# Kernel optimization log

Measured on AMD Instinct MI355X. Metric: run time of the kernel, lower is better.

The kernel has to match this reference:

```python
import jax, jax.numpy as jnp
import numpy as np
from jax import lax

V, E, NL, NS, DC, EX = 32000, 1024, 4, 16, 4, 2
DI = EX * E          # 2048 inner dim
DTR = E // 16        # 64 dt_rank
BSZ, L = 2, 512
EPS = 1e-5


def setup_inputs() -> dict:
    key = jax.random.key(0)
    ks = jax.random.split(key, 12)
    s = 0.02
    emb = jax.random.normal(ks[0], (V, E), jnp.float32) * s
    ln_w = jnp.ones((NL, E), jnp.float32)
    ln_b = jnp.zeros((NL, E), jnp.float32)
    in_proj_w = jax.random.normal(ks[1], (NL, 2 * DI, E), jnp.float32) * s
    conv_w = jax.random.normal(ks[2], (NL, DI, DC), jnp.float32) * 0.1
    conv_b = jnp.zeros((NL, DI), jnp.float32)
    x_proj_w = jax.random.normal(ks[3], (NL, DTR + 2 * NS, DI), jnp.float32) * s
    dt_proj_w = jax.random.normal(ks[4], (NL, DI, DTR), jnp.float32) * s
    dt_proj_b = jax.random.normal(ks[5], (NL, DI), jnp.float32) * 0.1
    # canonical S4D-real init: A[d,n] = n+1  ->  A_log = log(A)
    A_log = jnp.log(jnp.tile(jnp.arange(1, NS + 1, dtype=jnp.float32)[None, None, :], (NL, DI, 1)))
    D_param = jnp.ones((NL, DI), jnp.float32)
    out_proj_w = jax.random.normal(ks[6], (NL, E, DI), jnp.float32) * s
    fln_w = jnp.ones((E,), jnp.float32)
    fln_b = jnp.zeros((E,), jnp.float32)
    input_ids = jax.random.randint(ks[7], (BSZ, L), 0, V, jnp.int64)
    targets = jax.random.randint(ks[8], (BSZ, L), 0, V, jnp.int64)
    return dict(input_ids=input_ids, targets=targets, emb=emb, ln_w=ln_w, ln_b=ln_b,
                in_proj_w=in_proj_w, conv_w=conv_w, conv_b=conv_b, x_proj_w=x_proj_w,
                dt_proj_w=dt_proj_w, dt_proj_b=dt_proj_b, A_log=A_log, D_param=D_param,
                out_proj_w=out_proj_w, fln_w=fln_w, fln_b=fln_b)


def _layer_norm(x, w, b):
    mu = x.mean(-1, keepdims=True)
    var = ((x - mu) ** 2).mean(-1, keepdims=True)
    return (x - mu) * lax.rsqrt(var + EPS) * w + b


def _mamba_block(x, in_w, cw, cb, xw, dtw, dtb, a_log, d_par, ow):
    # x: (B,L,E)
    xz = jnp.einsum('ble,fe->blf', x, in_w)          # (B,L,2*DI)
    u, res = jnp.split(xz, 2, axis=-1)               # each (B,L,DI)
    # causal depthwise conv1d, kernel width DC (left pad DC-1)
    u_pad = jnp.pad(u, ((0, 0), (DC - 1, 0), (0, 0)))
    u_conv = sum(cw[:, k] * u_pad[:, k:k + u.shape[1], :] for k in range(DC))
    u = jax.nn.silu(u_conv + cb)
    x_dbl = jnp.einsum('bld,fd->blf', u, xw)         # (B,L,DTR+2*NS)
    dt = x_dbl[..., :DTR]
    Bm = x_dbl[..., DTR:DTR + NS]                    # (B,L,NS)
    Cm = x_dbl[..., DTR + NS:]                       # (B,L,NS)
    delta = jax.nn.softplus(jnp.einsum('blr,dr->bld', dt, dtw) + dtb)  # (B,L,DI)
    A = -jnp.exp(a_log)                              # (DI,NS)
    dA = jnp.exp(delta[..., None] * A)               # (B,L,DI,NS)
    dBu = delta[..., None] * Bm[:, :, None, :] * u[..., None]

    def step(h, inp):
        dA_t, dBu_t, C_t = inp
        h = dA_t * h + dBu_t                         # (B,DI,NS)
        y = jnp.einsum('bdn,bn->bd', h, C_t)
        return h, y

    h0 = jnp.zeros((x.shape[0], DI, NS), x.dtype)
    _, ys = lax.scan(step, h0, (dA.transpose(1, 0, 2, 3), dBu.transpose(1, 0, 2, 3), Cm.transpose(1, 0, 2)))
    y = ys.transpose(1, 0, 2) + u * d_par            # (B,L,DI)
    y = y * jax.nn.silu(res)
    return jnp.einsum('bld,ed->ble', y, ow)


def reference(input_ids, targets, emb, ln_w, ln_b, in_proj_w, conv_w, conv_b,
              x_proj_w, dt_proj_w, dt_proj_b, A_log, D_param, out_proj_w, fln_w, fln_b):
    x = emb[input_ids]                               # (B,L,E)
    for l in range(NL):
        h = _layer_norm(x, ln_w[l], ln_b[l])
        h = _mamba_block(h, in_proj_w[l], conv_w[l], conv_b[l], x_proj_w[l],
                         dt_proj_w[l], dt_proj_b[l], A_log[l], D_param[l], out_proj_w[l])
        x = x + h
    x = _layer_norm(x, fln_w, fln_b)
    logits = jnp.einsum('ble,ve->blv', x, emb)       # tied lm_head
    logp = jax.nn.log_softmax(logits, axis=-1)
    valid = targets != -1
    safe_t = jnp.where(valid, targets, 0)
    nll = -jnp.take_along_axis(logp, safe_t[..., None], axis=-1)[..., 0]
    loss = jnp.where(valid, nll, 0.0).mean()
    return logits, loss
```

## Files before the change

kernel.cpp:

```cpp
#include <hip/hip_runtime.h>
#include <cstdint>
#include <cstddef>

#define L_SEQ 512
#define NBATCH 2
#define NTOK 1024
#define E_DIM 1024
#define V_DIM 32000
#define DI_DIM 2048
#define NS_DIM 16
#define DTR_DIM 64
#define DC_DIM 4
#define NL_DIM 4
#define NC 8
#define LC (L_SEQ / NC)

typedef __bf16 bf16;
typedef __bf16 bf16x8 __attribute__((ext_vector_type(8)));
typedef __bf16 bf16x4 __attribute__((ext_vector_type(4)));
typedef float  f32x4  __attribute__((ext_vector_type(4)));

__device__ __forceinline__ void gload_lds16(const void* g, void* l)
{
    __builtin_amdgcn_global_load_lds((const __attribute__((address_space(1))) uint32_t*)g,
                                     (__attribute__((address_space(3))) uint32_t*)l, 16, 0, 0);
}

__device__ __forceinline__ float softplusf(float z)
{
    return fmaxf(z, 0.0f) + log1pf(expf(-fabsf(z)));
}

__global__ void cast_f32_to_bf16(const float* __restrict__ in, bf16* __restrict__ out, int n4)
{
    int stride = gridDim.x * blockDim.x;
    for (int i = blockIdx.x * blockDim.x + threadIdx.x; i < n4; i += stride) {
        f32x4 v = ((const f32x4*)in)[i];
        bf16x4 o;
        o[0] = (bf16)v[0]; o[1] = (bf16)v[1]; o[2] = (bf16)v[2]; o[3] = (bf16)v[3];
        ((bf16x4*)out)[i] = o;
    }
}

__global__ void cast3_kernel(const float* __restrict__ a, bf16* __restrict__ oa, int na4,
                             const float* __restrict__ b, bf16* __restrict__ ob, int nb4,
                             const float* __restrict__ c, bf16* __restrict__ oc, int nc4)
{
    int stride = gridDim.x * blockDim.x;
    int tot = na4 + nb4 + nc4;
    for (int i = blockIdx.x * blockDim.x + threadIdx.x; i < tot; i += stride) {
        const float* src; bf16* dst; int k = i;
        if (k < na4) { src = a; dst = oa; }
        else if ((k -= na4) < nb4) { src = b; dst = ob; }
        else { k -= nb4; src = c; dst = oc; }
        f32x4 v = ((const f32x4*)src)[k];
        bf16x4 o;
        o[0] = (bf16)v[0]; o[1] = (bf16)v[1]; o[2] = (bf16)v[2]; o[3] = (bf16)v[3];
        ((bf16x4*)dst)[k] = o;
    }
}

__global__ void embed_kernel(const int* __restrict__ ids, const float* __restrict__ emb,
                             float* __restrict__ x)
{
    int t = blockIdx.x;
    int id = ids[t];
    ((f32x4*)(x + (size_t)t * E_DIM))[threadIdx.x] =
        ((const f32x4*)(emb + (size_t)id * E_DIM))[threadIdx.x];
}

__global__ void ln_kernel(const float* __restrict__ x, const float* __restrict__ w,
                          const float* __restrict__ b, bf16* __restrict__ out)
{
    int t = blockIdx.x;
    int tid = threadIdx.x;
    f32x4 v = ((const f32x4*)(x + (size_t)t * E_DIM))[tid];
    float s  = v[0] + v[1] + v[2] + v[3];
    float sq = v[0]*v[0] + v[1]*v[1] + v[2]*v[2] + v[3]*v[3];
#pragma unroll
    for (int off = 1; off < 64; off <<= 1) { s += __shfl_xor(s, off); sq += __shfl_xor(sq, off); }
    __shared__ float ps[4], pq[4];
    if ((tid & 63) == 0) { ps[tid >> 6] = s; pq[tid >> 6] = sq; }
    __syncthreads();
    float S  = ps[0] + ps[1] + ps[2] + ps[3];
    float SQ = pq[0] + pq[1] + pq[2] + pq[3];
    float mu  = S * (1.0f / E_DIM);
    float var = SQ * (1.0f / E_DIM) - mu * mu;
    float rs  = rsqrtf(var + 1e-5f);
    f32x4 wv = ((const f32x4*)w)[tid];
    f32x4 bv = ((const f32x4*)b)[tid];
    bf16x4 o;
#pragma unroll
    for (int i = 0; i < 4; ++i) o[i] = (bf16)((v[i] - mu) * rs * wv[i] + bv[i]);
    ((bf16x4*)(out + (size_t)t * E_DIM))[tid] = o;
}

template<int BM, int BN, int BK, int MODE, int SK>
__global__ __launch_bounds__(256) void gemm_bt(const bf16* __restrict__ A, const bf16* __restrict__ B,
                                               void* __restrict__ Cv, int K,
                                               int lda, int ldb, int ldc,
                                               const float* __restrict__ bias,
                                               int RB, int CB, int CBpad)
{
    int pid = blockIdx.x;
    int per = RB * CBpad;
    int sk  = pid / per;
    int rem = pid - sk * per;
    int xcd = rem & 7;
    int j   = rem >> 3;
    int cpx = CBpad >> 3;
    int rb  = j % RB;
    int cb  = xcd * cpx + j / RB;
    if (cb >= CB) return;
    int kseg = K / SK;
    int kbeg = sk * kseg;
    int kend = kbeg + kseg;

    __shared__ __align__(16) bf16 As[BM * BK];
    __shared__ __align__(16) bf16 Bs[BN * BK];
    int tid  = threadIdx.x;
    int lane = tid & 63;
    int wid  = tid >> 6;
    int wr = wid >> 1, wc = wid & 1;
    int li = lane & 15, lg = lane >> 4;
    const bf16* Ablk = A + (size_t)(rb * BM) * lda;
    const bf16* Bblk = B + (size_t)(cb * BN) * ldb;
    constexpr int MR   = BM / 32;
    constexpr int NR   = BN / 32;
    constexpr int SEGS = BK / 8;
    constexpr int AOPS = BM * SEGS;
    constexpr int TOT  = (BM + BN) * SEGS;
    f32x4 acc[MR][NR] = {};
    for (int k0 = kbeg; k0 < kend; k0 += BK) {
        __syncthreads();
#pragma unroll
        for (int it = 0; it < TOT / 256; ++it) {
            int wbase = it * 256 + wid * 64;
            int idx   = wbase + lane;
            if (wbase < AOPS) {
                int row = idx / SEGS, seg = idx % SEGS;
                gload_lds16(Ablk + (size_t)row * lda + k0 + seg * 8, As + (size_t)wbase * 8);
            } else {
                int bb  = wbase - AOPS;
                int bi  = bb + lane;
                int row = bi / SEGS, seg = bi % SEGS;
                gload_lds16(Bblk + (size_t)row * ldb + k0 + seg * 8, Bs + (size_t)bb * 8);
            }
        }
        __syncthreads();
#pragma unroll
        for (int kk = 0; kk < BK / 32; ++kk) {
            bf16x8 af[MR], bfr[NR];
#pragma unroll
            for (int m = 0; m < MR; ++m)
                af[m]  = *(const bf16x8*)&As[(wr * (BM/2) + m * 16 + li) * BK + kk * 32 + lg * 8];
#pragma unroll
            for (int n = 0; n < NR; ++n)
                bfr[n] = *(const bf16x8*)&Bs[(wc * (BN/2) + n * 16 + li) * BK + kk * 32 + lg * 8];
#pragma unroll
            for (int m = 0; m < MR; ++m)
#pragma unroll
                for (int n = 0; n < NR; ++n)
                    acc[m][n] = __builtin_amdgcn_mfma_f32_16x16x32_bf16(af[m], bfr[n], acc[m][n], 0, 0, 0);
        }
    }
    int row0 = rb * BM + wr * (BM/2);
    int col0 = cb * BN + wc * (BN/2);
    float* Cf = (float*)Cv;
    bf16*  Cb = (bf16*)Cv;
#pragma unroll
    for (int m = 0; m < MR; ++m) {
#pragma unroll
        for (int n = 0; n < NR; ++n) {
            int r = row0 + m * 16 + lg * 4;
            int c = col0 + n * 16 + li;
#pragma unroll
            for (int q = 0; q < 4; ++q) {
                float v = acc[m][n][q];
                if (MODE == 0) {
                    Cf[(size_t)(r + q) * ldc + c] = v;
                } else if (MODE == 2) {
                    Cb[(size_t)(r + q) * ldc + c] = (bf16)softplusf(v + bias[c]);
                } else if (MODE == 4) {
                    Cb[(size_t)(r + q) * ldc + c] = (bf16)v;
                } else if (MODE == 5) {
                    atomicAdd(Cf + (size_t)(r + q) * ldc + c, v);
                }
            }
        }
    }
}

template<int BM, int BN, int BK, int MODE, int SK = 1>
static void launch_gemm(const bf16* A, const bf16* B, void* C, int M, int N, int K,
                        int lda, int ldb, int ldc, const float* bias, hipStream_t stream)
{
    int RB = M / BM;
    int CB = (N + BN - 1) / BN;
    int CBpad = (CB + 7) & ~7;
    gemm_bt<BM, BN, BK, MODE, SK><<<RB * CBpad * SK, 256, 0, stream>>>(A, B, C, K, lda, ldb, ldc,
                                                                       bias, RB, CB, CBpad);
}

__global__ __launch_bounds__(256) void cxk_kernel(
        const bf16* __restrict__ xz, const float* __restrict__ cw,
        const float* __restrict__ cb, const float* __restrict__ xw,
        float* __restrict__ xdbl, bf16* __restrict__ dt_bf, bf16* __restrict__ u_bf)
{
    int t0  = blockIdx.x * 4;
    int bb  = t0 >> 9;
    int tid = threadIdx.x;
    int f   = tid & 127;
    int ks  = tid >> 7;
    __shared__ __align__(16) float sxz[7][256];
    __shared__ __align__(16) float su[4][256];
    __shared__ float pacc[4][128];
    float acc[4] = {0, 0, 0, 0};
    for (int kc = 0; kc < DI_DIM; kc += 256) {
        __syncthreads();
        if (tid < 224) {
            int row = tid >> 5, c8 = (tid & 31) * 8;
            int tr = t0 - 3 + row;
            float vals[8] = {0, 0, 0, 0, 0, 0, 0, 0};
            if (tr >= bb * L_SEQ) {
                bf16x8 v = *(const bf16x8*)&xz[(size_t)tr * (2 * DI_DIM) + kc + c8];
#pragma unroll
                for (int jj = 0; jj < 8; ++jj) vals[jj] = (float)v[jj];
            }
#pragma unroll
            for (int jj = 0; jj < 8; ++jj) sxz[row][c8 + jj] = vals[jj];
        }
        __syncthreads();
        {
            int c = tid;
            const float* cwp = cw + (size_t)(kc + c) * DC_DIM;
            float w0 = cwp[0], w1 = cwp[1], w2 = cwp[2], w3 = cwp[3];
            float bs = cb[kc + c];
#pragma unroll
            for (int tt = 0; tt < 4; ++tt) {
                float a = bs + w0 * sxz[tt][c] + w1 * sxz[tt + 1][c]
                             + w2 * sxz[tt + 2][c] + w3 * sxz[tt + 3][c];
                float uo = a / (1.0f + __expf(-a));
                su[tt][c] = uo;
                u_bf[(size_t)(t0 + tt) * DI_DIM + kc + c] = (bf16)uo;
            }
        }
        __syncthreads();
        if (f < 96) {
            int kb = ks * 128;
            for (int kk = kb; kk < kb + 128; kk += 4) {
                f32x4 wv = *(const f32x4*)&xw[(size_t)f * DI_DIM + kc + kk];
#pragma unroll
                for (int tt = 0; tt < 4; ++tt) {
                    f32x4 uv = *(f32x4*)&su[tt][kk];
                    acc[tt] += wv[0]*uv[0] + wv[1]*uv[1] + wv[2]*uv[2] + wv[3]*uv[3];
                }
            }
        }
    }
    if (ks == 1 && f < 96) {
#pragma unroll
        for (int tt = 0; tt < 4; ++tt) pacc[tt][f] = acc[tt];
    }
    __syncthreads();
    if (ks == 0 && f < 96) {
#pragma unroll
        for (int tt = 0; tt < 4; ++tt) {
            float v = acc[tt] + pacc[tt][f];
            xdbl[(size_t)(t0 + tt) * 96 + f] = v;
            if (f < 64) dt_bf[(size_t)(t0 + tt) * DTR_DIM + f] = (bf16)v;
        }
    }
}

__global__ __launch_bounds__(256) void scan_phase_a(
        const bf16* __restrict__ delta, const float* __restrict__ xdbl,
        const bf16* __restrict__ u_bf, const float* __restrict__ A_log,
        float* __restrict__ Pbuf, float* __restrict__ Sbuf)
{
    int tid = threadIdx.x;
    int c   = blockIdx.x & (NC - 1);
    int dblk= (blockIdx.x >> 3) & 127;
    int b   = blockIdx.x >> 10;
    int d0  = dblk << 4;
    int n = tid & 15, dl = tid >> 4;
    int d = d0 + dl;
    float Ac = -expf(A_log[(size_t)d * NS_DIM + n]);
    float h = 0.0f, P = 1.0f;
    __shared__ float s_dlt[32][16], s_u[32][16], s_B[32][16];
    int tt0 = tid >> 4, cc = tid & 15;
    int tbase = b * L_SEQ + c * LC;
    for (int t0 = 0; t0 < LC; t0 += 32) {
        __syncthreads();
#pragma unroll
        for (int jj = 0; jj < 2; ++jj) {
            int tt = jj * 16 + tt0;
            size_t trow = (size_t)(tbase + t0 + tt);
            s_dlt[tt][cc] = (float)delta[trow * DI_DIM + d0 + cc];
            s_u[tt][cc]   = (float)u_bf[trow * DI_DIM + d0 + cc];
            s_B[tt][cc]   = xdbl[trow * 96 + 64 + cc];
        }
        __syncthreads();
#pragma unroll
        for (int t = 0; t < 32; ++t) {
            float dlt = s_dlt[t][dl];
            float dA  = __expf(dlt * Ac);
            h = fmaf(dA, h, dlt * s_B[t][n] * s_u[t][dl]);
            P *= dA;
        }
    }
    size_t oi = (((size_t)(b * NC + c) * DI_DIM) + d) * NS_DIM + n;
    Pbuf[oi] = P;
    Sbuf[oi] = h;
}

__global__ __launch_bounds__(256) void scan_phase_c(
        const bf16* __restrict__ delta, const float* __restrict__ xdbl,
        const bf16* __restrict__ u_bf, const bf16* __restrict__ xz,
        const float* __restrict__ A_log, const float* __restrict__ D_par,
        const float* __restrict__ Pbuf, const float* __restrict__ Sbuf,
        bf16* __restrict__ y)
{
    int tid = threadIdx.x;
    int c   = blockIdx.x & (NC - 1);
    int dblk= (blockIdx.x >> 3) & 127;
    int b   = blockIdx.x >> 10;
    int d0  = dblk << 4;
    int n = tid & 15, dl = tid >> 4;
    int d = d0 + dl;
    float Ac = -expf(A_log[(size_t)d * NS_DIM + n]);
    float Dp = D_par[d];
    float h = 0.0f;
    for (int cp = 0; cp < c; ++cp) {
        size_t oi = (((size_t)(b * NC + cp) * DI_DIM) + d) * NS_DIM + n;
        h = fmaf(Pbuf[oi], h, Sbuf[oi]);
    }
    __shared__ float s_dlt[32][16], s_u[32][16], s_res[32][16], s_B[32][16], s_C[32][16];
    __shared__ bf16  s_y[32][16];
    int tt0 = tid >> 4, cc = tid & 15;
    int tbase = b * L_SEQ + c * LC;
    for (int t0 = 0; t0 < LC; t0 += 32) {
        __syncthreads();
#pragma unroll
        for (int jj = 0; jj < 2; ++jj) {
            int tt = jj * 16 + tt0;
            size_t trow = (size_t)(tbase + t0 + tt);
            s_dlt[tt][cc] = (float)delta[trow * DI_DIM + d0 + cc];
            s_u[tt][cc]   = (float)u_bf[trow * DI_DIM + d0 + cc];
            s_res[tt][cc] = (float)xz[trow * (2 * DI_DIM) + DI_DIM + d0 + cc];
            s_B[tt][cc]   = xdbl[trow * 96 + 64 + cc];
            s_C[tt][cc]   = xdbl[trow * 96 + 80 + cc];
        }
        __syncthreads();
#pragma unroll
        for (int t = 0; t < 32; ++t) {
            float dlt = s_dlt[t][dl];
            float uu  = s_u[t][dl];
            float dA  = __expf(dlt * Ac);
            float dBu = dlt * s_B[t][n] * uu;
            h = fmaf(dA, h, dBu);
            float yp = h * s_C[t][n];
            yp += __shfl_xor(yp, 1);
            yp += __shfl_xor(yp, 2);
            yp += __shfl_xor(yp, 4);
            yp += __shfl_xor(yp, 8);
            if (n == 0) {
                float res = s_res[t][dl];
                float yv  = fmaf(uu, Dp, yp) * (res / (1.0f + __expf(-res)));
                s_y[t][dl] = (bf16)yv;
            }
        }
        __syncthreads();
#pragma unroll
        for (int jj = 0; jj < 2; ++jj) {
            int tt = jj * 16 + tt0;
            size_t trow = (size_t)(tbase + t0 + tt);
            y[trow * DI_DIM + d0 + cc] = s_y[tt][cc];
        }
    }
}

__global__ void lse_nll_kernel(const float* __restrict__ logits, const int* __restrict__ targets,
                               float* __restrict__ lossp)
{
    int t = blockIdx.x, tid = threadIdx.x;
    const f32x4* row = (const f32x4*)(logits + (size_t)t * V_DIM);
    float m = -1e30f, s = 0.0f;
    for (int i = tid; i < V_DIM / 4; i += 256) {
        f32x4 v = row[i];
        float m4 = fmaxf(fmaxf(v[0], v[1]), fmaxf(v[2], v[3]));
        if (m4 > m) { s *= __expf(m - m4); m = m4; }
        s += __expf(v[0] - m) + __expf(v[1] - m) + __expf(v[2] - m) + __expf(v[3] - m);
    }
#pragma unroll
    for (int off = 1; off < 64; off <<= 1) {
        float mo = __shfl_xor(m, off), so = __shfl_xor(s, off);
        float nm = fmaxf(m, mo);
        s = s * __expf(m - nm) + so * __expf(mo - nm);
        m = nm;
    }
    __shared__ float pm[4], ps2[4];
    if ((tid & 63) == 0) { pm[tid >> 6] = m; ps2[tid >> 6] = s; }
    __syncthreads();
    if (tid == 0) {
        float M = fmaxf(fmaxf(pm[0], pm[1]), fmaxf(pm[2], pm[3]));
        float S = ps2[0] * __expf(pm[0] - M) + ps2[1] * __expf(pm[1] - M)
                + ps2[2] * __expf(pm[2] - M) + ps2[3] * __expf(pm[3] - M);
        int tg = targets[t];
        if (tg >= 0) {
            float v = (M + logf(S)) - logits[(size_t)t * V_DIM + tg];
            atomicAdd(lossp, v * (1.0f / NTOK));
        }
    }
}

extern "C" void kernel_launch(void* const* d_in, const int* in_sizes, int n_in,
                              void* d_out, int out_size, void* d_ws, size_t ws_size,
                              hipStream_t stream)
{
    const int*   ids   = (const int*)d_in[0];
    const int*   tgt   = (const int*)d_in[1];
    const float* emb   = (const float*)d_in[2];
    const float* ln_w  = (const float*)d_in[3];
    const float* ln_b  = (const float*)d_in[4];
    const float* inw   = (const float*)d_in[5];
    const float* convw = (const float*)d_in[6];
    const float* convb = (const float*)d_in[7];
    const float* xw    = (const float*)d_in[8];
    const float* dtw   = (const float*)d_in[9];
    const float* dtb   = (const float*)d_in[10];
    const float* alog  = (const float*)d_in[11];
    const float* dpar  = (const float*)d_in[12];
    const float* outw  = (const float*)d_in[13];
    const float* flnw  = (const float*)d_in[14];
    const float* flnb  = (const float*)d_in[15];
    float* logits = (float*)d_out;
    float* lossp  = logits + (size_t)NTOK * V_DIM;

    const size_t INW_L  = (size_t)2 * DI_DIM * E_DIM;
    const size_t OUTW_L = (size_t)E_DIM * DI_DIM;
    const size_t DTW_L  = (size_t)DI_DIM * DTR_DIM;

    char* wsp = (char*)d_ws;
    size_t off = 0;
    auto alloc = [&](size_t bytes) -> void* {
        void* p = wsp + off;
        off += (bytes + 255) & ~(size_t)255;
        return p;
    };
    bf16*  emb_bf  = (bf16*)alloc((size_t)V_DIM * E_DIM * 2);
    float* x       = (float*)alloc((size_t)NTOK * E_DIM * 4);
    bf16*  h_bf    = (bf16*)alloc((size_t)NTOK * E_DIM * 2);
    bf16*  xzb     = (bf16*)alloc((size_t)NTOK * 2 * DI_DIM * 2);
    bf16*  u_bf    = (bf16*)alloc((size_t)NTOK * DI_DIM * 2);
    float* xdbl    = (float*)alloc((size_t)NTOK * 96 * 4);
    bf16*  dt_bf   = (bf16*)alloc((size_t)NTOK * DTR_DIM * 2);
    bf16*  deltab  = (bf16*)alloc((size_t)NTOK * DI_DIM * 2);
    bf16*  y_bf    = (bf16*)alloc((size_t)NTOK * DI_DIM * 2);
    bf16*  xf_bf   = (bf16*)alloc((size_t)NTOK * E_DIM * 2);
    float* Pbuf    = (float*)alloc((size_t)NBATCH * NC * DI_DIM * NS_DIM * 4);
    float* Sbuf    = (float*)alloc((size_t)NBATCH * NC * DI_DIM * NS_DIM * 4);
    size_t base = off;
    size_t big_need = base + (((size_t)NL_DIM * INW_L * 2 + 255) & ~(size_t)255)
                           + (((size_t)NL_DIM * OUTW_L * 2 + 255) & ~(size_t)255)
                           + (((size_t)NL_DIM * DTW_L * 2 + 255) & ~(size_t)255);
    bool big = (big_need <= ws_size);
    bf16* winl; bf16* woutl; bf16* wdtl;
    if (big) {
        winl  = (bf16*)alloc((size_t)NL_DIM * INW_L * 2);
        woutl = (bf16*)alloc((size_t)NL_DIM * OUTW_L * 2);
        wdtl  = (bf16*)alloc((size_t)NL_DIM * DTW_L * 2);
    } else {
        winl  = (bf16*)alloc(INW_L * 2);
        woutl = (bf16*)alloc(OUTW_L * 2);
        wdtl  = (bf16*)alloc(DTW_L * 2);
    }
    if (off > ws_size) return;

    hipMemsetAsync(lossp, 0, sizeof(float), stream);
    {
        int n4 = (int)((size_t)V_DIM * E_DIM / 4);
        cast_f32_to_bf16<<<4096, 256, 0, stream>>>(emb, emb_bf, n4);
    }
    if (big) {
        cast3_kernel<<<4096, 256, 0, stream>>>(
            inw,  winl,  (int)((size_t)NL_DIM * INW_L / 4),
            outw, woutl, (int)((size_t)NL_DIM * OUTW_L / 4),
            dtw,  wdtl,  (int)((size_t)NL_DIM * DTW_L / 4));
    }
    embed_kernel<<<NTOK, 256, 0, stream>>>(ids, emb, x);

    for (int l = 0; l < NL_DIM; ++l) {
        const bf16* wi = big ? winl  + (size_t)l * INW_L  : winl;
        const bf16* wo = big ? woutl + (size_t)l * OUTW_L : woutl;
        const bf16* wd = big ? wdtl  + (size_t)l * DTW_L  : wdtl;
        if (!big) {
            cast3_kernel<<<2048, 256, 0, stream>>>(
                inw  + (size_t)l * INW_L,  winl,  (int)(INW_L / 4),
                outw + (size_t)l * OUTW_L, woutl, (int)(OUTW_L / 4),
                dtw  + (size_t)l * DTW_L,  wdtl,  (int)(DTW_L / 4));
        }
        ln_kernel<<<NTOK, 256, 0, stream>>>(x, ln_w + l * E_DIM, ln_b + l * E_DIM, h_bf);
        launch_gemm<128, 64, 64, 4>(h_bf, wi, xzb, NTOK, 2 * DI_DIM, E_DIM,
                                    E_DIM, E_DIM, 2 * DI_DIM, nullptr, stream);
        cxk_kernel<<<NTOK / 4, 256, 0, stream>>>(
            xzb, convw + (size_t)l * DI_DIM * DC_DIM, convb + (size_t)l * DI_DIM,
            xw + (size_t)l * 96 * DI_DIM, xdbl, dt_bf, u_bf);
        launch_gemm<64, 64, 64, 2>(dt_bf, wd, deltab, NTOK, DI_DIM, DTR_DIM,
                                   DTR_DIM, DTR_DIM, DI_DIM, dtb + (size_t)l * DI_DIM, stream);
        scan_phase_a<<<NBATCH * (DI_DIM / 16) * NC, 256, 0, stream>>>(
            deltab, xdbl, u_bf, alog + (size_t)l * DI_DIM * NS_DIM, Pbuf, Sbuf);
        scan_phase_c<<<NBATCH * (DI_DIM / 16) * NC, 256, 0, stream>>>(
            deltab, xdbl, u_bf, xzb, alog + (size_t)l * DI_DIM * NS_DIM,
            dpar + (size_t)l * DI_DIM, Pbuf, Sbuf, y_bf);
        launch_gemm<128, 128, 64, 5, 4>(y_bf, wo, x, NTOK, E_DIM, DI_DIM,
                                        DI_DIM, DI_DIM, E_DIM, nullptr, stream);
    }
    ln_kernel<<<NTOK, 256, 0, stream>>>(x, flnw, flnb, xf_bf);
    launch_gemm<128, 128, 64, 0>(xf_bf, emb_bf, logits, NTOK, V_DIM, E_DIM,
                                 E_DIM, E_DIM, V_DIM, nullptr, stream);
    lse_nll_kernel<<<NTOK, 256, 0, stream>>>(logits, tgt, lossp);
}
```

Baseline: 857.9 us.

## Add dedicated 256x256-tile logits GEMM and shrink K-tile of layer GEMMs

Replaces the generic logits GEMM with a specialized 512-thread kernel that computes 256x256 output tiles. It uses double-buffered LDS staging via direct global-to-LDS loads, XOR swizzling, and a custom block-to-tile mapping over the 125 column blocks. The layer GEMMs switch their K tile from 64 to 32, which lowers LDS use and may raise occupancy at the cost of more loop iterations and syncs. The large tile gives more reuse per LDS load for the dominant vocab projection, but it needs 128 KB of LDS and many accumulator registers per thread.

```diff
diff --git a/kernel.cpp b/kernel.cpp
--- a/kernel.cpp
+++ b/kernel.cpp
@@ -200,6 +200,98 @@
     int CBpad = (CB + 7) & ~7;
     gemm_bt<BM, BN, BK, MODE, SK><<<RB * CBpad * SK, 256, 0, stream>>>(A, B, C, K, lda, ldb, ldc,
                                                                        bias, RB, CB, CBpad);
+}
+
+__global__ __launch_bounds__(512) void gemm256_logits(const bf16* __restrict__ A,
+                                                      const bf16* __restrict__ B,
+                                                      float* __restrict__ C)
+{
+    int pid = blockIdx.x;
+    int x = pid & 7, i = pid >> 3;
+    int cbq = (x < 5) ? 16 : 15;
+    int ci = i >> 2;
+    if (ci >= cbq) return;
+    int cb = (x < 5) ? x * 16 + ci : 80 + (x - 5) * 15 + ci;
+    int rb = i & 3;
+
+    __shared__ __align__(16) bf16 Abuf[2][256 * 64];
+    __shared__ __align__(16) bf16 Bbuf[2][256 * 64];
+    int tid  = threadIdx.x;
+    int lane = tid & 63, wid = tid >> 6;
+    int wr = wid >> 2, wc = wid & 3;
+    int li = lane & 15, lg = lane >> 4;
+    const bf16* Ablk = A + (size_t)(rb * 256) * E_DIM;
+    const bf16* Bblk = B + (size_t)(cb * 256) * E_DIM;
+
+    f32x4 acc[8][4] = {};
+
+    auto stage = [&](int buf, int k0) {
+#pragma unroll
+        for (int sw = 0; sw < 4; ++sw) {
+            int wb  = sw * 8192 + wid * 1024;
+            int y   = wb + lane * 16;
+            int row = y >> 7;
+            int colb = (y & 127) ^ ((row & 4) << 3);
+            gload_lds16(Ablk + (size_t)row * E_DIM + k0 + (colb >> 1),
+                        (char*)Abuf[buf] + wb);
+        }
+#pragma unroll
+        for (int sw = 0; sw < 4; ++sw) {
+            int wb  = sw * 8192 + wid * 1024;
+            int y   = wb + lane * 16;
+            int row = y >> 7;
+            int colb = (y & 127) ^ ((row & 4) << 3);
+            gload_lds16(Bblk + (size_t)row * E_DIM + k0 + (colb >> 1),
+                        (char*)Bbuf[buf] + wb);
+        }
+    };
+
+    stage(0, 0);
+    __syncthreads();
+    int cur = 0;
+    for (int t = 0; t < E_DIM / 64; ++t) {
+        if (t + 1 < E_DIM / 64) stage(cur ^ 1, (t + 1) * 64);
+        const char* Ab = (const char*)Abuf[cur];
+        const char* Bb = (const char*)Bbuf[cur];
+#pragma unroll
+        for (int kk = 0; kk < 2; ++kk) {
+            bf16x8 af[8], bfr[4];
+#pragma unroll
+            for (int m = 0; m < 8; ++m) {
+                int row = wr * 128 + m * 16 + li;
+                int ab  = ((row << 7) + kk * 64 + lg * 16) ^ ((li & 4) << 3);
+                af[m] = *(const bf16x8*)(Ab + ab);
+            }
+#pragma unroll
+            for (int n = 0; n < 4; ++n) {
+                int row = wc * 64 + n * 16 + li;
+                int bb  = ((row << 7) + kk * 64 + lg * 16) ^ ((li & 4) << 3);
+                bfr[n] = *(const bf16x8*)(Bb + bb);
+            }
+            __builtin_amdgcn_s_setprio(1);
+#pragma unroll
+            for (int m = 0; m < 8; ++m)
+#pragma unroll
+                for (int n = 0; n < 4; ++n)
+                    acc[m][n] = __builtin_amdgcn_mfma_f32_16x16x32_bf16(af[m], bfr[n], acc[m][n], 0, 0, 0);
+            __builtin_amdgcn_s_setprio(0);
+        }
+        __syncthreads();
+        cur ^= 1;
+    }
+    int row0 = rb * 256 + wr * 128;
+    int col0 = cb * 256 + wc * 64;
+#pragma unroll
+    for (int m = 0; m < 8; ++m) {
+#pragma unroll
+        for (int n = 0; n < 4; ++n) {
+            int r = row0 + m * 16 + lg * 4;
+            int c = col0 + n * 16 + li;
+#pragma unroll
+            for (int q = 0; q < 4; ++q)
+                C[(size_t)(r + q) * V_DIM + c] = acc[m][n][q];
+        }
+    }
 }
 
 __global__ __launch_bounds__(256) void cxk_kernel(
@@ -501,23 +593,22 @@
                 dtw  + (size_t)l * DTW_L,  wdtl,  (int)(DTW_L / 4));
         }
         ln_kernel<<<NTOK, 256, 0, stream>>>(x, ln_w + l * E_DIM, ln_b + l * E_DIM, h_bf);
-        launch_gemm<128, 64, 64, 4>(h_bf, wi, xzb, NTOK, 2 * DI_DIM, E_DIM,
+        launch_gemm<128, 64, 32, 4>(h_bf, wi, xzb, NTOK, 2 * DI_DIM, E_DIM,
                                     E_DIM, E_DIM, 2 * DI_DIM, nullptr, stream);
         cxk_kernel<<<NTOK / 4, 256, 0, stream>>>(
             xzb, convw + (size_t)l * DI_DIM * DC_DIM, convb + (size_t)l * DI_DIM,
             xw + (size_t)l * 96 * DI_DIM, xdbl, dt_bf, u_bf);
-        launch_gemm<64, 64, 64, 2>(dt_bf, wd, deltab, NTOK, DI_DIM, DTR_DIM,
+        launch_gemm<64, 64, 32, 2>(dt_bf, wd, deltab, NTOK, DI_DIM, DTR_DIM,
                                    DTR_DIM, DTR_DIM, DI_DIM, dtb + (size_t)l * DI_DIM, stream);
         scan_phase_a<<<NBATCH * (DI_DIM / 16) * NC, 256, 0, stream>>>(
             deltab, xdbl, u_bf, alog + (size_t)l * DI_DIM * NS_DIM, Pbuf, Sbuf);
         scan_phase_c<<<NBATCH * (DI_DIM / 16) * NC, 256, 0, stream>>>(
             deltab, xdbl, u_bf, xzb, alog + (size_t)l * DI_DIM * NS_DIM,
             dpar + (size_t)l * DI_DIM, Pbuf, Sbuf, y_bf);
-        launch_gemm<128, 128, 64, 5, 4>(y_bf, wo, x, NTOK, E_DIM, DI_DIM,
+        launch_gemm<128, 128, 32, 5, 4>(y_bf, wo, x, NTOK, E_DIM, DI_DIM,
                                         DI_DIM, DI_DIM, E_DIM, nullptr, stream);
     }
     ln_kernel<<<NTOK, 256, 0, stream>>>(x, flnw, flnb, xf_bf);
-    launch_gemm<128, 128, 64, 0>(xf_bf, emb_bf, logits, NTOK, V_DIM, E_DIM,
-                                 E_DIM, E_DIM, V_DIM, nullptr, stream);
+    gemm256_logits<<<512, 512, 0, stream>>>(xf_bf, emb_bf, logits);
     lse_nll_kernel<<<NTOK, 256, 0, stream>>>(logits, tgt, lossp);
 }
```

New measurement: 845.8 us. Within noise of the previous version (-1.4%).
